# Optimization experiments

Measured on AMD Instinct MI355X. Metric: run time of the kernel, lower is better.

The kernel has to match this reference:

```python
import jax, jax.numpy as jnp
import numpy as np

N_HEAD = 16
NEG_INF = -1e30


def sparsemax(z):
    # sparsemax over last axis (Martins & Astudillo 2016)
    d = z.shape[-1]
    z_sorted = -jnp.sort(-z, axis=-1)                      # descending
    z_cumsum = jnp.cumsum(z_sorted, axis=-1)
    k = jnp.arange(1, d + 1, dtype=z.dtype)
    support = (1.0 + k * z_sorted) > z_cumsum
    rho = jnp.sum(support, axis=-1, keepdims=True)         # int, >=1
    rho_idx = jnp.clip(rho - 1, 0, None).astype(jnp.int32)
    cs_at_rho = jnp.take_along_axis(z_cumsum, rho_idx, axis=-1)
    tau = (cs_at_rho - 1.0) / jnp.maximum(rho.astype(z.dtype), 1.0)
    return jnp.clip(z - tau, 0.0, None)


def setup_inputs() -> dict:
    key = jax.random.key(0)
    ks = jax.random.split(key, 5)
    B, T, C = 4, 2048, 1024
    x = jax.random.normal(ks[0], (B, T, C), dtype=jnp.float32)
    W_attn = jax.random.normal(ks[1], (C, 3 * C), dtype=jnp.float32) * (1.0 / np.sqrt(C))
    b_attn = jax.random.normal(ks[2], (3 * C,), dtype=jnp.float32) * 0.01
    W_proj = jax.random.normal(ks[3], (C, C), dtype=jnp.float32) * (1.0 / np.sqrt(C))
    b_proj = jax.random.normal(ks[4], (C,), dtype=jnp.float32) * 0.01
    return {"x": x, "W_attn": W_attn, "b_attn": b_attn, "W_proj": W_proj, "b_proj": b_proj}


def reference(x, W_attn, b_attn, W_proj, b_proj):
    B, T, C = x.shape
    H = N_HEAD
    D = C // H
    qkv = x @ W_attn + b_attn                               # [B,T,3C]
    q, k, v = jnp.split(qkv, 3, axis=-1)
    q = q.reshape(B, T, H, D).transpose(0, 2, 1, 3)         # [B,H,T,D]
    k = k.reshape(B, T, H, D).transpose(0, 2, 1, 3)
    v = v.reshape(B, T, H, D).transpose(0, 2, 1, 3)
    # sparsemax over head dim of K (mode xsa_sparsemax_k)
    k = sparsemax(k)
    att = jnp.einsum('bhqd,bhkd->bhqk', q, k) * (1.0 / np.sqrt(D))
    causal = jnp.tril(jnp.ones((T, T), dtype=bool))
    att = jnp.where(causal[None, None], att, NEG_INF)
    att = jax.nn.softmax(att, axis=-1)
    y = jnp.einsum('bhqk,bhkd->bhqd', att, v)               # [B,H,T,D]
    # XSA output correction: subtract projection of y onto normalized v
    v_norm = jnp.sqrt(jnp.sum(v * v, axis=-1, keepdims=True))
    v_hat = v / jnp.maximum(v_norm, 1e-12)
    proj_coef = jnp.sum(y * v_hat, axis=-1, keepdims=True)
    y = y - proj_coef * v_hat
    y = y.transpose(0, 2, 1, 3).reshape(B, T, C)
    return y @ W_proj + b_proj
```

## Files before the change

kernel.cpp:

```cpp
#include <hip/hip_runtime.h>
#include <math.h>

#define NB 4
#define NH 16
#define TT 2048
#define CC 1024
#define DD 64
#define MM (NB * TT)
#define BK 32

typedef __attribute__((ext_vector_type(8))) _Float16 half8;
typedef __attribute__((ext_vector_type(4))) _Float16 half4;
typedef __attribute__((ext_vector_type(4))) float floatx4;

__device__ __forceinline__ void gload16(const _Float16* g, _Float16* l) {
    auto gp = (const __attribute__((address_space(1))) void*)(uintptr_t)g;
    auto lp = (__attribute__((address_space(3))) void*)(uint32_t)(uintptr_t)l;
    __builtin_amdgcn_global_load_lds(gp, lp, 16, 0, 0);
}

__global__ __launch_bounds__(256) void split_x_kernel(
    const float* __restrict__ x, _Float16* __restrict__ xh,
    _Float16* __restrict__ xl)
{
    size_t i = ((size_t)blockIdx.x * 256 + threadIdx.x) * 4;
    float4 v = *(const float4*)&x[i];
    half4 h, l;
    h.x = (_Float16)v.x; l.x = (_Float16)(v.x - (float)h.x);
    h.y = (_Float16)v.y; l.y = (_Float16)(v.y - (float)h.y);
    h.z = (_Float16)v.z; l.z = (_Float16)(v.z - (float)h.z);
    h.w = (_Float16)v.w; l.w = (_Float16)(v.w - (float)h.w);
    *(half4*)&xh[i] = h;
    *(half4*)&xl[i] = l;
}

__global__ __launch_bounds__(256) void splitT_w_kernel(
    const float* __restrict__ W, _Float16* __restrict__ WhT,
    _Float16* __restrict__ WlT, int K, int N)
{
    __shared__ float Ls[64][65];
    const int bN = blockIdx.x * 64;
    const int bK = blockIdx.y * 64;
    const int tid = threadIdx.x;
    const int g = tid >> 4, c = tid & 15;

    #pragma unroll
    for (int u = 0; u < 4; u++) {
        int r = u * 16 + g;
        float4 v = *(const float4*)&W[(size_t)(bK + r) * N + bN + c * 4];
        Ls[r][c * 4 + 0] = v.x; Ls[r][c * 4 + 1] = v.y;
        Ls[r][c * 4 + 2] = v.z; Ls[r][c * 4 + 3] = v.w;
    }
    __syncthreads();
    #pragma unroll
    for (int u = 0; u < 4; u++) {
        int n = u * 16 + g;
        half4 h, l;
        float f;
        f = Ls[c * 4 + 0][n]; h.x = (_Float16)f; l.x = (_Float16)(f - (float)h.x);
        f = Ls[c * 4 + 1][n]; h.y = (_Float16)f; l.y = (_Float16)(f - (float)h.y);
        f = Ls[c * 4 + 2][n]; h.z = (_Float16)f; l.z = (_Float16)(f - (float)h.z);
        f = Ls[c * 4 + 3][n]; h.w = (_Float16)f; l.w = (_Float16)(f - (float)h.w);
        size_t o = (size_t)(bN + n) * K + bK + c * 4;
        *(half4*)&WhT[o] = h;
        *(half4*)&WlT[o] = l;
    }
}

__global__ __launch_bounds__(512, 2) void gemm_ht3_kernel(
    const _Float16* __restrict__ Ah, const _Float16* __restrict__ Al,
    const _Float16* __restrict__ Bh, const _Float16* __restrict__ Bl,
    const float* __restrict__ bias, float* __restrict__ Cout,
    _Float16* __restrict__ outQh, _Float16* __restrict__ outQl,
    _Float16* __restrict__ outKh, _Float16* __restrict__ outKl,
    _Float16* __restrict__ outVt, int N, int K, int nbx, int mode)
{
    __shared__ _Float16 sAh[3][128 * BK], sAl[3][128 * BK];
    __shared__ _Float16 sBh[3][256 * BK], sBl[3][256 * BK];

    const int nblk = gridDim.x;
    const int id = blockIdx.x;
    const int swzid = (id & 7) * (nblk >> 3) + (id >> 3);
    const int by = swzid / nbx, bx = swzid - by * nbx;
    const int bm = by * 128, bn = bx * 256;

    const int tid = threadIdx.x;
    const int w = tid >> 6, lane = tid & 63;
    const int wm = (w >> 2) * 64, wn = (w & 3) * 64;
    const int fr = lane & 15, g = lane >> 4;

    const int rS = w * 16 + (lane >> 2);
    const int ug = ((lane & 3) ^ ((rS >> 1) & 3)) * 8;
    const size_t gA  = (size_t)(bm + rS) * K + ug;
    const size_t gB0 = (size_t)(bn + rS) * K + ug;
    const size_t gB1 = (size_t)(bn + 128 + rS) * K + ug;
    const int ldsW = w * 16 * BK;

    auto stage = [&](int kt, int c) {
        const int k0 = kt * BK;
        gload16(&Ah[gA + k0],  &sAh[c][ldsW]);
        gload16(&Al[gA + k0],  &sAl[c][ldsW]);
        gload16(&Bh[gB0 + k0], &sBh[c][ldsW]);
        gload16(&Bl[gB0 + k0], &sBl[c][ldsW]);
        gload16(&Bh[gB1 + k0], &sBh[c][128 * BK + ldsW]);
        gload16(&Bl[gB1 + k0], &sBl[c][128 * BK + ldsW]);
    };

    int offA[4], offB[4];
    #pragma unroll
    for (int t = 0; t < 4; t++) {
        const int ra = wm + t * 16 + fr;
        offA[t] = ra * BK + ((g ^ ((ra >> 1) & 3)) << 3);
        const int rb = wn + t * 16 + fr;
        offB[t] = rb * BK + ((g ^ ((rb >> 1) & 3)) << 3);
    }

    floatx4 acc[4][4];
    #pragma unroll
    for (int i = 0; i < 4; i++)
        #pragma unroll
        for (int j = 0; j < 4; j++)
            acc[i][j] = (floatx4){0.f, 0.f, 0.f, 0.f};

    stage(0, 0);
    stage(1, 1);
    stage(2, 2);
    asm volatile("s_waitcnt vmcnt(12)" ::: "memory");
    __builtin_amdgcn_sched_barrier(0);
    __builtin_amdgcn_s_barrier();

    const int NK = K >> 5;
    int b3 = 0;
    for (int kt = 0; kt < NK; kt++) {
        half8 a_h[4], a_l[4], b_h[4], b_l[4];
        #pragma unroll
        for (int t = 0; t < 4; t++) {
            a_h[t] = *(const half8*)&sAh[b3][offA[t]];
            a_l[t] = *(const half8*)&sAl[b3][offA[t]];
            b_h[t] = *(const half8*)&sBh[b3][offB[t]];
            b_l[t] = *(const half8*)&sBl[b3][offB[t]];
        }
        __builtin_amdgcn_s_setprio(1);
        #pragma unroll
        for (int mt = 0; mt < 4; mt++)
            #pragma unroll
            for (int nt = 0; nt < 4; nt++) {
                acc[mt][nt] = __builtin_amdgcn_mfma_f32_16x16x32_f16(
                    a_h[mt], b_h[nt], acc[mt][nt], 0, 0, 0);
                acc[mt][nt] = __builtin_amdgcn_mfma_f32_16x16x32_f16(
                    a_h[mt], b_l[nt], acc[mt][nt], 0, 0, 0);
                acc[mt][nt] = __builtin_amdgcn_mfma_f32_16x16x32_f16(
                    a_l[mt], b_h[nt], acc[mt][nt], 0, 0, 0);
            }
        __builtin_amdgcn_s_setprio(0);
        __builtin_amdgcn_sched_barrier(0);
        __builtin_amdgcn_s_barrier();
        if (kt + 3 < NK) {
            stage(kt + 3, b3);
            asm volatile("s_waitcnt vmcnt(12)" ::: "memory");
        } else if (kt + 3 == NK) {
            asm volatile("s_waitcnt vmcnt(6)" ::: "memory");
        } else if (kt + 2 == NK) {
            asm volatile("s_waitcnt vmcnt(0)" ::: "memory");
        }
        __builtin_amdgcn_sched_barrier(0);
        __builtin_amdgcn_s_barrier();
        b3 = (b3 == 2) ? 0 : b3 + 1;
    }

    const int col = lane & 15, row4 = g * 4;
    if (mode == 0) {
        #pragma unroll
        for (int mt = 0; mt < 4; mt++)
            #pragma unroll
            for (int nt = 0; nt < 4; nt++) {
                const int n = bn + wn + nt * 16 + col;
                const float bv = bias[n];
                const int m0 = bm + wm + mt * 16 + row4;
                #pragma unroll
                for (int r = 0; r < 4; r++)
                    Cout[(size_t)(m0 + r) * N + n] = acc[mt][nt][r] + bv;
            }
    } else {
        #pragma unroll
        for (int mt = 0; mt < 4; mt++)
            #pragma unroll
            for (int nt = 0; nt < 4; nt++) {
                const int n = bn + wn + nt * 16 + col;
                const int which = n >> 10;
                const int cc_ = n & 1023;
                const int hh_ = cc_ >> 6, d = cc_ & 63;
                const int m0 = bm + wm + mt * 16 + row4;
                const int b = m0 >> 11, t0 = m0 & 2047;
                const size_t bhx = (size_t)b * NH + hh_;
                const float bv = bias[n];
                if (which == 0) {
                    #pragma unroll
                    for (int r = 0; r < 4; r++) {
                        const float qv = (acc[mt][nt][r] + bv) * 0.125f;
                        const _Float16 qh_ = (_Float16)qv;
                        const size_t o = (bhx * TT + t0 + r) * DD + d;
                        outQh[o] = qh_;
                        outQl[o] = (_Float16)(qv - (float)qh_);
                    }
                } else if (which == 1) {
                    #pragma unroll
                    for (int r = 0; r < 4; r++) {
                        const float kv = acc[mt][nt][r] + bv;
                        const _Float16 kh_ = (_Float16)kv;
                        const size_t o = (bhx * TT + t0 + r) * DD + d;
                        outKh[o] = kh_;
                        outKl[o] = (_Float16)(kv - (float)kh_);
                    }
                } else {
                    half4 vv;
                    #pragma unroll
                    for (int r = 0; r < 4; r++)
                        vv[r] = (_Float16)(acc[mt][nt][r] + bv);
                    *(half4*)&outVt[(bhx * DD + d) * TT + t0] = vv;
                }
            }
    }
}

__global__ __launch_bounds__(256) void sparsemax_kernel(
    _Float16* __restrict__ Kh, _Float16* __restrict__ Kl)
{
    const int lane = threadIdx.x & 63;
    const size_t row = (size_t)blockIdx.x * 4 + (threadIdx.x >> 6);
    const size_t off = row * DD + lane;
    float z = (float)Kh[off] + (float)Kl[off];
    float cnt = 0.f, ss = 0.f;
    #pragma unroll
    for (int j = 0; j < 64; j++) {
        float zj = __shfl(z, j, 64);
        if (zj >= z) { cnt += 1.f; ss += zj; }
    }
    float cond = (1.f + cnt * z > ss) ? 1.f : 0.f;
    float rho = cond, S = cond * z;
    #pragma unroll
    for (int o = 32; o; o >>= 1) {
        rho += __shfl_xor(rho, o, 64);
        S   += __shfl_xor(S,   o, 64);
    }
    float tau = (S - 1.f) / rho;
    float outv = fmaxf(z - tau, 0.f);
    _Float16 hh = (_Float16)outv;
    Kh[off] = hh;
    Kl[off] = (_Float16)(outv - (float)hh);
}

__global__ __launch_bounds__(256, 2) void attn_kernel(
    const _Float16* __restrict__ Qh, const _Float16* __restrict__ Ql,
    const _Float16* __restrict__ Kh, const _Float16* __restrict__ Kl,
    const _Float16* __restrict__ Vt,
    _Float16* __restrict__ Yh, _Float16* __restrict__ Yl)
{
    __shared__ _Float16 sKh[2][64 * DD];
    __shared__ _Float16 sKl[2][64 * DD];
    __shared__ _Float16 sV [2][64 * DD];

    const int tid = threadIdx.x;
    const int w = tid >> 6, lane = tid & 63;
    const int p = blockIdx.x >> 6;
    const int bhid = blockIdx.x & 63;
    const int b = bhid >> 4, h = bhid & 15;
    const size_t bh = (size_t)b * NH + h;
    const _Float16* Qhg = Qh + bh * (size_t)TT * DD;
    const _Float16* Qlg = Ql + bh * (size_t)TT * DD;
    const _Float16* Khg = Kh + bh * (size_t)TT * DD;
    const _Float16* Klg = Kl + bh * (size_t)TT * DD;
    const _Float16* Vtg = Vt + bh * (size_t)DD * TT;

    const int qrow = lane & 15;
    const int g = lane >> 4;
    const int swz = qrow & 7;
    const int sr = lane >> 3;
    const int uu = (lane & 7) ^ sr;

    auto stage = [&](int kt, int buf) {
        const int rb = w * 16;
        #pragma unroll
        for (int i = 0; i < 2; i++) {
            const int rr = rb + i * 8 + sr;
            const size_t ko = (size_t)(kt * 64 + rr) * DD + (uu << 3);
            gload16(&Khg[ko], &sKh[buf][(rb + i * 8) * DD]);
            gload16(&Klg[ko], &sKl[buf][(rb + i * 8) * DD]);
            gload16(&Vtg[(size_t)rr * TT + kt * 64 + (uu << 3)],
                    &sV[buf][(rb + i * 8) * DD]);
        }
    };

    const int qlist[2] = {p, 15 - p};
    int cur = 0;

    for (int qi = 0; qi < 2; qi++) {
        const int qt = qlist[qi];
        const int wq0 = qt * 128 + w * 32;
        const int wqmax = wq0 + 31;
        const int nkv = 2 * qt + 2;

        half8 qfh[2][2], qfl[2][2];
        #pragma unroll
        for (int nq = 0; nq < 2; nq++)
            #pragma unroll
            for (int ks = 0; ks < 2; ks++) {
                const size_t o = (size_t)(wq0 + nq * 16 + qrow) * DD
                               + (g << 3) + (ks << 5);
                qfh[nq][ks] = *(const half8*)&Qhg[o];
                qfl[nq][ks] = *(const half8*)&Qlg[o];
            }

        floatx4 acc[2][4];
        #pragma unroll
        for (int i = 0; i < 2; i++)
            #pragma unroll
            for (int j = 0; j < 4; j++)
                acc[i][j] = (floatx4){0.f, 0.f, 0.f, 0.f};
        float m_i[2] = {-3.0e38f, -3.0e38f};
        float l_i[2] = {0.f, 0.f};

        __syncthreads();
        stage(0, cur);

        for (int kt = 0; kt < nkv; kt++) {
            __syncthreads();
            if (kt + 1 < nkv) stage(kt + 1, cur ^ 1);

            if (kt * 64 <= wqmax) {
                const _Float16* kb = sKh[cur];
                const _Float16* lb = sKl[cur];
                const _Float16* vbp = sV[cur];

                floatx4 s[4][2];
                #pragma unroll
                for (int mk = 0; mk < 4; mk++)
                    #pragma unroll
                    for (int nq = 0; nq < 2; nq++)
                        s[mk][nq] = (floatx4){0.f, 0.f, 0.f, 0.f};

                #pragma unroll
                for (int mk = 0; mk < 4; mk++) {
                    #pragma unroll
                    for (int ks = 0; ks < 2; ks++) {
                        const int off = (qrow + mk * 16) * DD
                                      + (((g + (ks << 2)) ^ swz) << 3);
                        const half8 kfh = *(const half8*)&kb[off];
                        const half8 kfl = *(const half8*)&lb[off];
                        #pragma unroll
                        for (int nq = 0; nq < 2; nq++) {
                            s[mk][nq] = __builtin_amdgcn_mfma_f32_16x16x32_f16(
                                kfh, qfh[nq][ks], s[mk][nq], 0, 0, 0);
                            s[mk][nq] = __builtin_amdgcn_mfma_f32_16x16x32_f16(
                                kfh, qfl[nq][ks], s[mk][nq], 0, 0, 0);
                            s[mk][nq] = __builtin_amdgcn_mfma_f32_16x16x32_f16(
                                kfl, qfh[nq][ks], s[mk][nq], 0, 0, 0);
                        }
                    }
                }

                if (kt * 64 + 63 > wq0) {
                    #pragma unroll
                    for (int mk = 0; mk < 4; mk++)
                        #pragma unroll
                        for (int nq = 0; nq < 2; nq++)
                            #pragma unroll
                            for (int r = 0; r < 4; r++) {
                                const int kvg = kt * 64 + mk * 16 + (g << 2) + r;
                                const int qg  = wq0 + nq * 16 + qrow;
                                if (kvg > qg) s[mk][nq][r] = -1.0e30f;
                            }
                }

                float al_[2];
                #pragma unroll
                for (int nq = 0; nq < 2; nq++) {
                    float mx = s[0][nq][0];
                    #pragma unroll
                    for (int mk = 0; mk < 4; mk++)
                        #pragma unroll
                        for (int r = 0; r < 4; r++)
                            mx = fmaxf(mx, s[mk][nq][r]);
                    mx = fmaxf(mx, __shfl_xor(mx, 16, 64));
                    mx = fmaxf(mx, __shfl_xor(mx, 32, 64));
                    const float mn = fmaxf(m_i[nq], mx);
                    al_[nq] = __expf(m_i[nq] - mn);
                    m_i[nq] = mn;
                    float r0 = 0.f;
                    #pragma unroll
                    for (int mk = 0; mk < 4; mk++)
                        #pragma unroll
                        for (int r = 0; r < 4; r++) {
                            const float pp = __expf(s[mk][nq][r] - mn);
                            s[mk][nq][r] = pp;
                            r0 += pp;
                        }
                    r0 += __shfl_xor(r0, 16, 64);
                    r0 += __shfl_xor(r0, 32, 64);
                    l_i[nq] = l_i[nq] * al_[nq] + r0;
                }

                #pragma unroll
                for (int mt = 0; mt < 2; mt++)
                    #pragma unroll
                    for (int r = 0; r < 4; r++) {
                        const float aB = __shfl(al_[mt], (g << 2) | r, 64);
                        #pragma unroll
                        for (int nt = 0; nt < 4; nt++)
                            acc[mt][nt][r] *= aB;
                    }

                half4 ph[4][2], pl[4][2];
                #pragma unroll
                for (int mk = 0; mk < 4; mk++)
                    #pragma unroll
                    for (int nq = 0; nq < 2; nq++)
                        #pragma unroll
                        for (int r = 0; r < 4; r++) {
                            const float pv = s[mk][nq][r];
                            const _Float16 hh = (_Float16)pv;
                            ph[mk][nq][r] = hh;
                            pl[mk][nq][r] = (_Float16)(pv - (float)hh);
                        }

                #pragma unroll
                for (int mk = 0; mk < 4; mk++) {
                    #pragma unroll
                    for (int nt = 0; nt < 4; nt++) {
                        const int d = qrow + nt * 16;
                        const int u = ((mk << 1) | (g >> 1)) ^ swz;
                        const half4 vb = *(const half4*)
                            &vbp[d * DD + (u << 3) + ((g & 1) << 2)];
                        #pragma unroll
                        for (int nq = 0; nq < 2; nq++) {
                            acc[nq][nt] = __builtin_amdgcn_mfma_f32_16x16x16f16(
                                ph[mk][nq], vb, acc[nq][nt], 0, 0, 0);
                            acc[nq][nt] = __builtin_amdgcn_mfma_f32_16x16x16f16(
                                pl[mk][nq], vb, acc[nq][nt], 0, 0, 0);
                        }
                    }
                }
            }
            cur ^= 1;
        }

        #pragma unroll
        for (int mt = 0; mt < 2; mt++)
            #pragma unroll
            for (int r = 0; r < 4; r++) {
                const int qg = wq0 + mt * 16 + (g << 2) + r;
                const float invl = 1.0f / __shfl(l_i[mt], (g << 2) | r, 64);
                float y0 = acc[mt][0][r] * invl;
                float y1 = acc[mt][1][r] * invl;
                float y2 = acc[mt][2][r] * invl;
                float y3 = acc[mt][3][r] * invl;
                const float v0 = (float)Vtg[(size_t)qrow * TT + qg];
                const float v1 = (float)Vtg[(size_t)(qrow + 16) * TT + qg];
                const float v2 = (float)Vtg[(size_t)(qrow + 32) * TT + qg];
                const float v3 = (float)Vtg[(size_t)(qrow + 48) * TT + qg];
                float n2 = v0 * v0 + v1 * v1 + v2 * v2 + v3 * v3;
                #pragma unroll
                for (int o = 8; o; o >>= 1) n2 += __shfl_xor(n2, o, 64);
                const float ivn = 1.0f / fmaxf(sqrtf(n2), 1e-12f);
                float coef = y0 * v0 + y1 * v1 + y2 * v2 + y3 * v3;
                #pragma unroll
                for (int o = 8; o; o >>= 1) coef += __shfl_xor(coef, o, 64);
                coef *= ivn * ivn;
                const float o0 = y0 - coef * v0;
                const float o1 = y1 - coef * v1;
                const float o2 = y2 - coef * v2;
                const float o3 = y3 - coef * v3;
                const size_t ob = ((size_t)(b * TT + qg)) * CC + h * DD + qrow;
                _Float16 hh;
                hh = (_Float16)o0; Yh[ob]      = hh; Yl[ob]      = (_Float16)(o0 - (float)hh);
                hh = (_Float16)o1; Yh[ob + 16] = hh; Yl[ob + 16] = (_Float16)(o1 - (float)hh);
                hh = (_Float16)o2; Yh[ob + 32] = hh; Yl[ob + 32] = (_Float16)(o2 - (float)hh);
                hh = (_Float16)o3; Yh[ob + 48] = hh; Yl[ob + 48] = (_Float16)(o3 - (float)hh);
            }
    }
}

extern "C" void kernel_launch(void* const* d_in, const int* in_sizes, int n_in,
                              void* d_out, int out_size, void* d_ws, size_t ws_size,
                              hipStream_t stream) {
    const float* x      = (const float*)d_in[0];
    const float* W_attn = (const float*)d_in[1];
    const float* b_attn = (const float*)d_in[2];
    const float* W_proj = (const float*)d_in[3];
    const float* b_proj = (const float*)d_in[4];
    float* out = (float*)d_out;

    char* ws = (char*)d_ws;
    _Float16* xh   = (_Float16*)(ws);
    _Float16* xl   = (_Float16*)(ws + ((size_t)16 << 20));
    _Float16* WhT  = (_Float16*)(ws + ((size_t)32 << 20));
    _Float16* WlT  = (_Float16*)(ws + ((size_t)38 << 20));
    _Float16* Qh_  = (_Float16*)(ws + ((size_t)44 << 20));
    _Float16* Ql_  = (_Float16*)(ws + ((size_t)60 << 20));
    _Float16* Kh_  = (_Float16*)(ws + ((size_t)76 << 20));
    _Float16* Kl_  = (_Float16*)(ws + ((size_t)92 << 20));
    _Float16* Vt_  = (_Float16*)(ws + ((size_t)108 << 20));
    _Float16* Yh   = xh;
    _Float16* Yl   = xl;
    _Float16* WphT = WhT;
    _Float16* WplT = (_Float16*)(ws + ((size_t)34 << 20));

    split_x_kernel<<<(MM * CC) / (256 * 4), 256, 0, stream>>>(x, xh, xl);
    splitT_w_kernel<<<dim3(3 * CC / 64, CC / 64), 256, 0, stream>>>(
        W_attn, WhT, WlT, CC, 3 * CC);
    gemm_ht3_kernel<<<dim3((MM / 128) * (3 * CC / 256)), 512, 0, stream>>>(
        xh, xl, WhT, WlT, b_attn, nullptr,
        Qh_, Ql_, Kh_, Kl_, Vt_, 3 * CC, CC, 3 * CC / 256, 1);
    sparsemax_kernel<<<dim3((NB * NH * TT) / 4), 256, 0, stream>>>(Kh_, Kl_);
    attn_kernel<<<dim3(512), 256, 0, stream>>>(Qh_, Ql_, Kh_, Kl_, Vt_, Yh, Yl);
    splitT_w_kernel<<<dim3(CC / 64, CC / 64), 256, 0, stream>>>(
        W_proj, WphT, WplT, CC, CC);
    gemm_ht3_kernel<<<dim3((MM / 128) * (CC / 256)), 512, 0, stream>>>(
        Yh, Yl, WphT, WplT, b_proj, out,
        nullptr, nullptr, nullptr, nullptr, nullptr, CC, CC, CC / 256, 0);
}
```

Baseline: 538.4 us.

## Split GEMM MFMA loop to overlap async global-to-LDS stage with compute

The split-fp16 GEMM main loop now reads LDS fragments with explicit ds_read_b128 inline asm and an lgkmcnt fence. The 48 MFMAs are split into two halves, with the prefetch of tile kt+3 issued between them right after the barrier. Previously all MFMAs finished before the stage was issued. The aim is to hide global_load_lds issue latency behind the second MFMA half. The inline asm limits compiler scheduling, and the full lgkm wait before any MFMA removes interleaving of LDS reads with compute.

```diff
diff --git a/kernel.cpp b/kernel.cpp
--- a/kernel.cpp
+++ b/kernel.cpp
@@ -17,6 +17,16 @@
     auto gp = (const __attribute__((address_space(1))) void*)(uintptr_t)g;
     auto lp = (__attribute__((address_space(3))) void*)(uint32_t)(uintptr_t)l;
     __builtin_amdgcn_global_load_lds(gp, lp, 16, 0, 0);
+}
+
+__device__ __forceinline__ half8 lds_read_b128(uint32_t addr) {
+    floatx4 r;
+    asm volatile("ds_read_b128 %0, %1" : "=v"(r) : "v"(addr));
+    return __builtin_bit_cast(half8, r);
+}
+__device__ __forceinline__ void lgkm_fence() {
+    asm volatile("s_waitcnt lgkmcnt(0)" ::: "memory");
+    __builtin_amdgcn_sched_barrier(0);
 }
 
 __global__ __launch_bounds__(256) void split_x_kernel(
@@ -106,13 +116,13 @@
         gload16(&Bl[gB1 + k0], &sBl[c][128 * BK + ldsW]);
     };
 
-    int offA[4], offB[4];
+    uint32_t offA[4], offB[4];
     #pragma unroll
     for (int t = 0; t < 4; t++) {
         const int ra = wm + t * 16 + fr;
-        offA[t] = ra * BK + ((g ^ ((ra >> 1) & 3)) << 3);
+        offA[t] = (uint32_t)(ra * BK + ((g ^ ((ra >> 1) & 3)) << 3)) * 2;
         const int rb = wn + t * 16 + fr;
-        offB[t] = rb * BK + ((g ^ ((rb >> 1) & 3)) << 3);
+        offB[t] = (uint32_t)(rb * BK + ((g ^ ((rb >> 1) & 3)) << 3)) * 2;
     }
 
     floatx4 acc[4][4];
@@ -132,19 +142,25 @@
     const int NK = K >> 5;
     int b3 = 0;
     for (int kt = 0; kt < NK; kt++) {
+        const uint32_t aAh = (uint32_t)(uintptr_t)&sAh[b3][0];
+        const uint32_t aAl = (uint32_t)(uintptr_t)&sAl[b3][0];
+        const uint32_t aBh = (uint32_t)(uintptr_t)&sBh[b3][0];
+        const uint32_t aBl = (uint32_t)(uintptr_t)&sBl[b3][0];
         half8 a_h[4], a_l[4], b_h[4], b_l[4];
         #pragma unroll
         for (int t = 0; t < 4; t++) {
-            a_h[t] = *(const half8*)&sAh[b3][offA[t]];
-            a_l[t] = *(const half8*)&sAl[b3][offA[t]];
-            b_h[t] = *(const half8*)&sBh[b3][offB[t]];
-            b_l[t] = *(const half8*)&sBl[b3][offB[t]];
+            a_h[t] = lds_read_b128(aAh + offA[t]);
+            a_l[t] = lds_read_b128(aAl + offA[t]);
+            b_h[t] = lds_read_b128(aBh + offB[t]);
+            b_l[t] = lds_read_b128(aBl + offB[t]);
         }
+        lgkm_fence();
+
         __builtin_amdgcn_s_setprio(1);
         #pragma unroll
         for (int mt = 0; mt < 4; mt++)
             #pragma unroll
-            for (int nt = 0; nt < 4; nt++) {
+            for (int nt = 0; nt < 2; nt++) {
                 acc[mt][nt] = __builtin_amdgcn_mfma_f32_16x16x32_f16(
                     a_h[mt], b_h[nt], acc[mt][nt], 0, 0, 0);
                 acc[mt][nt] = __builtin_amdgcn_mfma_f32_16x16x32_f16(
@@ -153,16 +169,30 @@
                     a_l[mt], b_h[nt], acc[mt][nt], 0, 0, 0);
             }
         __builtin_amdgcn_s_setprio(0);
-        __builtin_amdgcn_sched_barrier(0);
         __builtin_amdgcn_s_barrier();
-        if (kt + 3 < NK) {
-            stage(kt + 3, b3);
+
+        if (kt + 3 < NK) stage(kt + 3, b3);
+
+        __builtin_amdgcn_s_setprio(1);
+        #pragma unroll
+        for (int mt = 0; mt < 4; mt++)
+            #pragma unroll
+            for (int nt = 2; nt < 4; nt++) {
+                acc[mt][nt] = __builtin_amdgcn_mfma_f32_16x16x32_f16(
+                    a_h[mt], b_h[nt], acc[mt][nt], 0, 0, 0);
+                acc[mt][nt] = __builtin_amdgcn_mfma_f32_16x16x32_f16(
+                    a_h[mt], b_l[nt], acc[mt][nt], 0, 0, 0);
+                acc[mt][nt] = __builtin_amdgcn_mfma_f32_16x16x32_f16(
+                    a_l[mt], b_h[nt], acc[mt][nt], 0, 0, 0);
+            }
+        __builtin_amdgcn_s_setprio(0);
+
+        if (kt + 3 < NK)
             asm volatile("s_waitcnt vmcnt(12)" ::: "memory");
-        } else if (kt + 3 == NK) {
+        else if (kt + 3 == NK)
             asm volatile("s_waitcnt vmcnt(6)" ::: "memory");
-        } else if (kt + 2 == NK) {
+        else if (kt + 2 == NK)
             asm volatile("s_waitcnt vmcnt(0)" ::: "memory");
-        }
         __builtin_amdgcn_sched_barrier(0);
         __builtin_amdgcn_s_barrier();
         b3 = (b3 == 2) ? 0 : b3 + 1;
```

Result: faster. 527.1 us (-2.1%).
